# Kernel optimization log

Hardware: AMD Instinct MI355X
Metric: run time of the kernel (lower is better)

Reference implementation:

```python
import jax, jax.numpy as jnp
import numpy as np

MIN_DEPTH = 0.1   # BaseConfig.MIN_DEPTH (assumed)
MAX_DEPTH = 100.0 # BaseConfig.MAX_DEPTH (assumed)
SIGMA = 0.5
KERNEL_SIZE = 3


def setup_inputs() -> dict:
    key = jax.random.key(0)
    k1, k2, k3, k4 = jax.random.split(key, 4)
    B, N = 8, 4096  # B = batch*views
    pred_depth = jax.random.uniform(k1, (B, N), jnp.float32, 0.5, 10.0)
    ray_3d = jax.random.normal(k2, (B, N, 3), jnp.float32)
    # Conv1d(1, 1, kernel_size=3) parameters: weight (out=1, in=1, k), bias (1,)
    fan_in = 1 * KERNEL_SIZE
    bound = 1.0 / np.sqrt(fan_in)
    conv_w = jax.random.uniform(k3, (1, 1, KERNEL_SIZE), jnp.float32, -bound, bound)
    conv_b = jax.random.uniform(k4, (1,), jnp.float32, -bound, bound)
    global_scale = jnp.ones((1,), jnp.float32)
    return {"pred_depth": pred_depth, "ray_3d": ray_3d,
            "conv_w": conv_w, "conv_b": conv_b, "global_scale": global_scale}


def reference(pred_depth, ray_3d, conv_w, conv_b, global_scale):
    # pred_depth: (B, N); ray_3d: (B, N, 3)
    scaled = pred_depth * global_scale  # global scale (broadcast scalar param)

    # Conv1d(1->1, k=3, padding=1) over the point axis. NCW / OIW layouts.
    x = scaled[:, None, :]  # (B, 1, N)
    pad = KERNEL_SIZE // 2
    sm = jax.lax.conv_general_dilated(
        x, conv_w, window_strides=(1,), padding=[(pad, pad)],
        dimension_numbers=("NCW", "OIW", "NCW"))
    smoothed = sm[:, 0, :] + conv_b  # (B, N)

    # Pairwise squared Euclidean distances (== cdist(..)**2), computed directly.
    sq = jnp.sum(ray_3d * ray_3d, axis=-1)  # (B, N)
    inner = jnp.einsum("bnd,bmd->bnm", ray_3d, ray_3d)  # (B, N, N)
    d2 = jnp.maximum(sq[:, :, None] + sq[:, None, :] - 2.0 * inner, 0.0)

    # Gaussian kernel weights and weighted depth aggregation (bmm).
    w = jnp.exp(-d2 / (2.0 * SIGMA * SIGMA))  # (B, N, N)
    weighted = jnp.einsum("bnm,bm->bn", w, smoothed)  # (B, N)

    return jnp.clip(weighted, MIN_DEPTH, MAX_DEPTH)
```

## Files before the change

kernel.cpp:

```cpp
#include <hip/hip_runtime.h>
#include <math.h>

#define NFULL 4096
#define BATCH 8
#define LOG2E 1.44269504088896340736f

#define GSPLIT 16
#define NPT 4
#define MC (NFULL / GSPLIT)

#if __has_builtin(__builtin_amdgcn_exp2f)
#define EXP2(x) __builtin_amdgcn_exp2f(x)
#else
#define EXP2(x) exp2f(x)
#endif

__global__ __launch_bounds__(256) void prep_kernel(
    const float* __restrict__ pred, const float* __restrict__ ray,
    const float* __restrict__ cw, const float* __restrict__ cb,
    const float* __restrict__ gs, float4* __restrict__ pm)
{
    int idx = blockIdx.x * 256 + threadIdx.x;
    int b = idx >> 12, n = idx & (NFULL - 1);
    float g  = gs[0];
    float w0 = cw[0], w1 = cw[1], w2 = cw[2], bias = cb[0];
    const float* pd = pred + b * NFULL;
    float pm1 = (n > 0)         ? pd[n - 1] : 0.f;
    float p0  = pd[n];
    float pp1 = (n < NFULL - 1) ? pd[n + 1] : 0.f;
    float sm = g * (w0 * pm1 + w1 * p0 + w2 * pp1) + bias;

    const float* r = ray + (size_t)idx * 3;
    float x = r[0], y = r[1], z = r[2];
    float sq = x * x + y * y + z * z;
    float sp = -2.f * LOG2E * sq;
    float shat = sm * EXP2(sp + 64.f);

    const float K = 2.4022448f;
    pm[idx] = make_float4(K * x, K * y, K * z, shat);
}

__global__ __launch_bounds__(256) void pairs_kernel(
    const float4* __restrict__ pm, float* __restrict__ partial)
{
    int tid  = threadIdx.x;
    int lane = tid & 63;
    int w    = blockIdx.x * 4 + (tid >> 6);
    int g  = w & (GSPLIT - 1);  w >>= 4;
    int nt = w & 15;            int b = w >> 4;

    const float4* P = pm + b * NFULL;
    int n0 = nt * 256 + lane;

    float4 a[NPT];
    float  Cn[NPT];
    float  acc[NPT];
#pragma unroll
    for (int k = 0; k < NPT; ++k) {
        a[k] = P[n0 + 64 * k];
        Cn[k] = -0.5f * (a[k].x * a[k].x + a[k].y * a[k].y + a[k].z * a[k].z) - 64.f;
        acc[k] = 0.f;
    }

    int m0 = g * MC;
#pragma unroll 4
    for (int m = m0; m < m0 + MC; ++m) {
        float4 q = P[m];
#pragma unroll
        for (int k = 0; k < NPT; ++k) {
            float t = fmaf(a[k].x, q.x, Cn[k]);
            t = fmaf(a[k].y, q.y, t);
            t = fmaf(a[k].z, q.z, t);
            acc[k] = fmaf(EXP2(t), q.w, acc[k]);
        }
    }

    float* outp = partial + (size_t)g * (BATCH * NFULL) + b * NFULL;
#pragma unroll
    for (int k = 0; k < NPT; ++k) outp[n0 + 64 * k] = acc[k];
}

__global__ __launch_bounds__(256) void reduce_kernel(
    const float* __restrict__ partial, float* __restrict__ out)
{
    int idx = blockIdx.x * 256 + threadIdx.x;
    float s = 0.f;
#pragma unroll
    for (int gg = 0; gg < GSPLIT; ++gg)
        s += partial[(size_t)gg * (BATCH * NFULL) + idx];
    out[idx] = fminf(fmaxf(s, 0.1f), 100.f);
}

extern "C" void kernel_launch(void* const* d_in, const int* in_sizes, int n_in,
                              void* d_out, int out_size, void* d_ws, size_t ws_size,
                              hipStream_t stream) {
    const float* pred = (const float*)d_in[0];
    const float* ray  = (const float*)d_in[1];
    const float* cw   = (const float*)d_in[2];
    const float* cb   = (const float*)d_in[3];
    const float* gs   = (const float*)d_in[4];
    float* out = (float*)d_out;

    float4* pm      = (float4*)d_ws;
    float*  partial = (float*)((char*)d_ws + (size_t)BATCH * NFULL * sizeof(float4));

    prep_kernel<<<BATCH * NFULL / 256, 256, 0, stream>>>(pred, ray, cw, cb, gs, pm);
    pairs_kernel<<<(BATCH * 16 * GSPLIT) / 4, 256, 0, stream>>>(pm, partial);
    reduce_kernel<<<BATCH * NFULL / 256, 256, 0, stream>>>(partial, out);
}
```

Before: 98.04 us.

## Use packed v2f FMAs in pair loop, double split, vectorize reduce

The pairwise Gaussian loop now keeps the four query points as two-wide float vectors so the distance FMAs can map to packed FP32 instructions, leaving only the exp2 calls scalar. GSPLIT is doubled to 32, which doubles the number of waves working on the m-range for better occupancy and latency hiding, and the inner unroll goes from 4 to 8. The reduce kernel reads and writes float4 to cut instruction count. In exchange the partial buffer and the reduce pass become twice as large, and the exp2 throughput still limits the inner loop.

```diff
diff --git a/kernel.cpp b/kernel.cpp
--- a/kernel.cpp
+++ b/kernel.cpp
@@ -5,9 +5,11 @@
 #define BATCH 8
 #define LOG2E 1.44269504088896340736f
 
-#define GSPLIT 16
+#define GSPLIT 32
 #define NPT 4
 #define MC (NFULL / GSPLIT)
+
+typedef float v2f __attribute__((ext_vector_type(2)));
 
 #if __has_builtin(__builtin_amdgcn_exp2f)
 #define EXP2(x) __builtin_amdgcn_exp2f(x)
@@ -46,49 +48,66 @@
     int tid  = threadIdx.x;
     int lane = tid & 63;
     int w    = blockIdx.x * 4 + (tid >> 6);
-    int g  = w & (GSPLIT - 1);  w >>= 4;
+    int g  = w & (GSPLIT - 1);  w >>= 5;
     int nt = w & 15;            int b = w >> 4;
 
     const float4* P = pm + b * NFULL;
     int n0 = nt * 256 + lane;
 
-    float4 a[NPT];
-    float  Cn[NPT];
-    float  acc[NPT];
+    v2f ax[2], ay[2], az[2], Cn[2], acc[2];
 #pragma unroll
-    for (int k = 0; k < NPT; ++k) {
-        a[k] = P[n0 + 64 * k];
-        Cn[k] = -0.5f * (a[k].x * a[k].x + a[k].y * a[k].y + a[k].z * a[k].z) - 64.f;
-        acc[k] = 0.f;
+    for (int p = 0; p < 2; ++p) {
+        float4 a0 = P[n0 + 64 * (2 * p)];
+        float4 a1 = P[n0 + 64 * (2 * p + 1)];
+        ax[p] = (v2f){a0.x, a1.x};
+        ay[p] = (v2f){a0.y, a1.y};
+        az[p] = (v2f){a0.z, a1.z};
+        v2f sq = __builtin_elementwise_fma(ax[p], ax[p],
+                 __builtin_elementwise_fma(ay[p], ay[p], az[p] * az[p]));
+        Cn[p] = -0.5f * sq - 64.f;
+        acc[p] = (v2f){0.f, 0.f};
     }
 
     int m0 = g * MC;
-#pragma unroll 4
+#pragma unroll 8
     for (int m = m0; m < m0 + MC; ++m) {
         float4 q = P[m];
+        v2f qx = (v2f){q.x, q.x}, qy = (v2f){q.y, q.y},
+            qz = (v2f){q.z, q.z}, qw = (v2f){q.w, q.w};
 #pragma unroll
-        for (int k = 0; k < NPT; ++k) {
-            float t = fmaf(a[k].x, q.x, Cn[k]);
-            t = fmaf(a[k].y, q.y, t);
-            t = fmaf(a[k].z, q.z, t);
-            acc[k] = fmaf(EXP2(t), q.w, acc[k]);
+        for (int p = 0; p < 2; ++p) {
+            v2f t = __builtin_elementwise_fma(ax[p], qx, Cn[p]);
+            t = __builtin_elementwise_fma(ay[p], qy, t);
+            t = __builtin_elementwise_fma(az[p], qz, t);
+            v2f e = (v2f){EXP2(t.x), EXP2(t.y)};
+            acc[p] = __builtin_elementwise_fma(e, qw, acc[p]);
         }
     }
 
     float* outp = partial + (size_t)g * (BATCH * NFULL) + b * NFULL;
 #pragma unroll
-    for (int k = 0; k < NPT; ++k) outp[n0 + 64 * k] = acc[k];
+    for (int p = 0; p < 2; ++p) {
+        outp[n0 + 64 * (2 * p)]     = acc[p].x;
+        outp[n0 + 64 * (2 * p + 1)] = acc[p].y;
+    }
 }
 
 __global__ __launch_bounds__(256) void reduce_kernel(
-    const float* __restrict__ partial, float* __restrict__ out)
+    const float4* __restrict__ partial, float4* __restrict__ out)
 {
     int idx = blockIdx.x * 256 + threadIdx.x;
-    float s = 0.f;
+    float4 s = make_float4(0.f, 0.f, 0.f, 0.f);
 #pragma unroll
-    for (int gg = 0; gg < GSPLIT; ++gg)
-        s += partial[(size_t)gg * (BATCH * NFULL) + idx];
-    out[idx] = fminf(fmaxf(s, 0.1f), 100.f);
+    for (int gg = 0; gg < GSPLIT; ++gg) {
+        float4 v = partial[(size_t)gg * (BATCH * NFULL / 4) + idx];
+        s.x += v.x; s.y += v.y; s.z += v.z; s.w += v.w;
+    }
+    float4 r;
+    r.x = fminf(fmaxf(s.x, 0.1f), 100.f);
+    r.y = fminf(fmaxf(s.y, 0.1f), 100.f);
+    r.z = fminf(fmaxf(s.z, 0.1f), 100.f);
+    r.w = fminf(fmaxf(s.w, 0.1f), 100.f);
+    out[idx] = r;
 }
 
 extern "C" void kernel_launch(void* const* d_in, const int* in_sizes, int n_in,
@@ -99,12 +118,12 @@
     const float* cw   = (const float*)d_in[2];
     const float* cb   = (const float*)d_in[3];
     const float* gs   = (const float*)d_in[4];
-    float* out = (float*)d_out;
 
     float4* pm      = (float4*)d_ws;
     float*  partial = (float*)((char*)d_ws + (size_t)BATCH * NFULL * sizeof(float4));
 
     prep_kernel<<<BATCH * NFULL / 256, 256, 0, stream>>>(pred, ray, cw, cb, gs, pm);
     pairs_kernel<<<(BATCH * 16 * GSPLIT) / 4, 256, 0, stream>>>(pm, partial);
-    reduce_kernel<<<BATCH * NFULL / 256, 256, 0, stream>>>(partial, out);
+    reduce_kernel<<<BATCH * NFULL / 1024, 256, 0, stream>>>(
+        (const float4*)partial, (float4*)d_out);
 }
```

Result: faster. 87.94 us (-10.3%).
